# Kernel optimization log

Hardware: AMD Instinct MI355X
Metric: run time of the kernel (lower is better)

The kernel has to match this reference:

```python
import jax, jax.numpy as jnp
import numpy as np

_EPS = 1e-6
_ATTN_WIDTH = 64  # must match init_kwargs


def setup_inputs() -> dict:
    key = jax.random.key(0)
    k1, k2, k3, k4 = jax.random.split(key, 4)
    N, C, L, D = 8, 64, 512, 64
    scale = 1.0 / np.sqrt(C)
    return {
        "x": jax.random.normal(k1, (N, C, L), dtype=jnp.float32),
        "Wx": jax.random.normal(k2, (C, D), dtype=jnp.float32) * scale,
        "Wt": jax.random.normal(k3, (C, D), dtype=jnp.float32) * scale,
        "bh": jnp.zeros((D,), dtype=jnp.float32),
        "Wa": jax.random.normal(k4, (D, 1), dtype=jnp.float32) * scale,
        "ba": jnp.zeros((1,), dtype=jnp.float32),
    }


def reference(x, Wx, Wt, bh, Wa, ba):
    # x: (N, C, L) -> (N, L, C)
    xt = jnp.transpose(x, (0, 2, 1))
    q = jnp.einsum("nlc,cd->nld", xt, Wt)  # query proj
    k = jnp.einsum("nlc,cd->nld", xt, Wx)  # key proj
    # additive (Bahdanau) scores: h is (N, L, L, D)
    h = jnp.tanh(q[:, :, None, :] + k[:, None, :, :] + bh)
    e = jnp.einsum("nijd,d->nij", h, Wa[:, 0]) + ba[0]  # (N, L, L)
    e = jnp.exp(e - jnp.max(e, axis=-1, keepdims=True))
    # banded mask: keep where -attn_width//2 <= j-i <= attn_width//2 - 1
    L = e.shape[-1]
    i = jnp.arange(L)[:, None]
    j = jnp.arange(L)[None, :]
    d = j - i
    mask = (d >= -(_ATTN_WIDTH // 2)) & (d <= _ATTN_WIDTH // 2 - 1)
    e = jnp.where(mask, e, 0.0)
    s = jnp.sum(e, axis=-1, keepdims=True)
    a = e / (s + _EPS)  # (N, L, L)
    v = jnp.einsum("nij,njc->nic", a, xt)  # (N, L, C)
    v = jnp.transpose(v, (0, 2, 1))  # (N, C, L)
    return (v, a)
```

## Files before the change

kernel.cpp:

```cpp
#include <hip/hip_runtime.h>

#define N_ 8
#define C_ 64
#define L_ 512
#define D_ 64
#define TI 8
#define JT 71
#define KST 68
#define XST 76
#define XBST 88
#define AST 76

#define C2F 2.8853900817779268f

typedef _Float16 f16x8 __attribute__((ext_vector_type(8)));
typedef float    f32x4 __attribute__((ext_vector_type(4)));

__device__ __forceinline__ float rcp_f(float x) { return __builtin_amdgcn_rcpf(x); }
__device__ __forceinline__ float ex2(float x)   { return __builtin_amdgcn_exp2f(x); }

__global__ __launch_bounds__(512, 4) void fused_kernel(
    const float* __restrict__ x, const float* __restrict__ Wx,
    const float* __restrict__ Wt, const float* __restrict__ bh,
    const float* __restrict__ Wa,
    float* __restrict__ vout, float* __restrict__ aout)
{
  __shared__ __attribute__((aligned(16))) float    xs[C_ * XST];
  __shared__ __attribute__((aligned(16))) _Float16 xb[80 * XBST];
  __shared__ __attribute__((aligned(16))) float    k2b[96 * KST];
  __shared__ float ash[TI * AST];
  __shared__ float vs[C_][9];

  const int tid  = threadIdx.x;
  const int lane = tid & 63;
  const int bx   = blockIdx.x;
  const int n    = bx & 7;
  const int t    = bx >> 3;
  const int i0   = t << 3;
  const int jbase = i0 - 32;

  for (int idx = tid; idx < C_ * 18; idx += 512) {
    int c = idx / 18, qq = idx - c * 18;
    int jj = qq << 2;
    int j = jbase + jj;
    float4 xv = {0.f, 0.f, 0.f, 0.f};
    if (j >= 0 && j < L_) xv = *(const float4*)(x + (n * C_ + c) * L_ + j);
    *(float4*)&xs[c * XST + jj] = xv;
    _Float16* xbp = xb + c;
    xbp[(jj + 0) * XBST] = (_Float16)(xv.x * C2F);
    xbp[(jj + 1) * XBST] = (_Float16)(xv.y * C2F);
    xbp[(jj + 2) * XBST] = (_Float16)(xv.z * C2F);
    xbp[(jj + 3) * XBST] = (_Float16)(xv.w * C2F);
  }
  __syncthreads();

  const int w = __builtin_amdgcn_readfirstlane(tid >> 6);

  if (w < 6) {
    const int abase = (w < 5) ? w * 16 : 32;
    const float* Wm = (w < 5) ? Wx : Wt;
    const int l15 = lane & 15, g = lane >> 4;
    const _Float16* ap = xb + (abase + l15) * XBST + g * 8;
    const f16x8 af0 = *(const f16x8*)(ap);
    const f16x8 af1 = *(const f16x8*)(ap + 32);
    const int drow = ((w < 5) ? w * 16 : 80) + g * 4;
    #pragma unroll
    for (int nt = 0; nt < 4; ++nt) {
      f32x4 acc = {0.f, 0.f, 0.f, 0.f};
      #pragma unroll
      for (int kk = 0; kk < 2; ++kk) {
        const float* bp = Wm + (g * 8 + kk * 32) * D_ + nt * 16 + l15;
        f16x8 bf;
        bf[0] = (_Float16)bp[0 * D_];
        bf[1] = (_Float16)bp[1 * D_];
        bf[2] = (_Float16)bp[2 * D_];
        bf[3] = (_Float16)bp[3 * D_];
        bf[4] = (_Float16)bp[4 * D_];
        bf[5] = (_Float16)bp[5 * D_];
        bf[6] = (_Float16)bp[6 * D_];
        bf[7] = (_Float16)bp[7 * D_];
        acc = __builtin_amdgcn_mfma_f32_16x16x32_f16(kk ? af1 : af0, bf, acc, 0, 0, 0);
      }
      float* dp = &k2b[drow * KST + nt * 16 + l15];
      dp[0 * KST] = acc[0];
      dp[1 * KST] = acc[1];
      dp[2 * KST] = acc[2];
      dp[3 * KST] = acc[3];
    }
  }
  __syncthreads();
  k2b[(80 + w) * KST + lane] += bh[lane] * C2F;
  __syncthreads();

  const int i = i0 + w;
  const float* kp = &k2b[(w + lane) * KST];
  const float* qp = &k2b[(80 + w) * KST];
  float a0 = 0.f, a1 = 0.f, a2 = 0.f, a3 = 0.f;
  #pragma unroll 4
  for (int dc = 0; dc < D_; dc += 4) {
    float4 kv = *(const float4*)(kp + dc);
    float4 qv = *(const float4*)(qp + dc);
    float4 wv = *(const float4*)(Wa + dc);
    a0 = fmaf(rcp_f(ex2(kv.x + qv.x) + 1.f), wv.x, a0);
    a1 = fmaf(rcp_f(ex2(kv.y + qv.y) + 1.f), wv.y, a1);
    a2 = fmaf(rcp_f(ex2(kv.z + qv.z) + 1.f), wv.z, a2);
    a3 = fmaf(rcp_f(ex2(kv.w + qv.w) + 1.f), wv.w, a3);
  }
  const float acc = (a0 + a1) + (a2 + a3);

  const int j = i - 32 + lane;
  const bool valid = (j >= 0) && (j < L_);
  float m = valid ? acc : 1e30f;
  #pragma unroll
  for (int off = 32; off; off >>= 1) m = fminf(m, __shfl_xor(m, off, 64));
  float p = valid ? ex2(C2F * (m - acc)) : 0.f;
  float s = p;
  #pragma unroll
  for (int off = 32; off; off >>= 1) s += __shfl_xor(s, off, 64);
  const float av = p * rcp_f(s + 1e-6f);

  float* arow_s = &ash[w * AST];
  arow_s[lane] = 0.f;
  if (lane < AST - 64) arow_s[64 + lane] = 0.f;
  arow_s[w + lane] = av;

  {
    const int src  = (lane - i + 32) & 63;
    const float ar = __shfl(av, src, 64);
    const int jsrc = i - 32 + src;
    const int seg  = (jsrc >= 0) ? (jsrc >> 6) : 9;
    float* arow = aout + (size_t)(n * L_ + i) * L_;
    #pragma unroll
    for (int s8 = 0; s8 < 8; ++s8)
      arow[s8 * 64 + lane] = (s8 == seg) ? ar : 0.f;
  }

  {
    const int qstart = w & ~3;
    float v = 0.f;
    const float* xp = &xs[lane * XST];
    #pragma unroll 4
    for (int tq = 0; tq < 17; ++tq) {
      const int jj = qstart + 4 * tq;
      float4 a4 = *(const float4*)(arow_s + jj);
      float4 xq = *(const float4*)(xp + jj);
      v = fmaf(a4.x, xq.x, v);
      v = fmaf(a4.y, xq.y, v);
      v = fmaf(a4.z, xq.z, v);
      v = fmaf(a4.w, xq.w, v);
    }
    vs[lane][w] = v;
  }
  __syncthreads();
  {
    int c = tid >> 3, il = tid & 7;
    vout[((size_t)n * C_ + c) * L_ + i0 + il] = vs[c][il];
  }
}

extern "C" void kernel_launch(void* const* d_in, const int* in_sizes, int n_in,
                              void* d_out, int out_size, void* d_ws, size_t ws_size,
                              hipStream_t stream) {
  const float* x  = (const float*)d_in[0];
  const float* Wx = (const float*)d_in[1];
  const float* Wt = (const float*)d_in[2];
  const float* bh = (const float*)d_in[3];
  const float* Wa = (const float*)d_in[4];
  (void)d_ws; (void)ws_size;

  float* vout = (float*)d_out;
  float* aout = vout + N_ * C_ * L_;

  fused_kernel<<<512, 512, 0, stream>>>(x, Wx, Wt, bh, Wa, vout, aout);
}
```

Measured before the change: 15.26 us.

## Spread projection MFMAs across all waves and prefetch weights before barrier

Drops the separate fp16 transposed staging buffer and builds MFMA A-fragments straight from the fp32 x tile in shared memory. The 24 projection tiles are spread evenly over all 8 waves, 3 per wave, instead of 4 tiles on each of 6 waves. Weight loads are issued before the first barrier so they overlap the x tile loads. The bias is folded into the accumulator init, which removes one barrier and one read-modify-write pass. The cost is more register pressure from the prefetched weights and strided scalar LDS reads for the A fragments.

```diff
diff --git a/kernel.cpp b/kernel.cpp
--- a/kernel.cpp
+++ b/kernel.cpp
@@ -5,10 +5,8 @@
 #define L_ 512
 #define D_ 64
 #define TI 8
-#define JT 71
 #define KST 68
-#define XST 76
-#define XBST 88
+#define XST 84
 #define AST 76
 
 #define C2F 2.8853900817779268f
@@ -25,9 +23,8 @@
     const float* __restrict__ Wa,
     float* __restrict__ vout, float* __restrict__ aout)
 {
-  __shared__ __attribute__((aligned(16))) float    xs[C_ * XST];
-  __shared__ __attribute__((aligned(16))) _Float16 xb[80 * XBST];
-  __shared__ __attribute__((aligned(16))) float    k2b[96 * KST];
+  __shared__ __attribute__((aligned(16))) float xs[C_ * XST];
+  __shared__ __attribute__((aligned(16))) float k2b[96 * KST];
   __shared__ float ash[TI * AST];
   __shared__ float vs[C_][9];
 
@@ -39,57 +36,78 @@
   const int i0   = t << 3;
   const int jbase = i0 - 32;
 
-  for (int idx = tid; idx < C_ * 18; idx += 512) {
-    int c = idx / 18, qq = idx - c * 18;
-    int jj = qq << 2;
-    int j = jbase + jj;
-    float4 xv = {0.f, 0.f, 0.f, 0.f};
-    if (j >= 0 && j < L_) xv = *(const float4*)(x + (n * C_ + c) * L_ + j);
-    *(float4*)&xs[c * XST + jj] = xv;
-    _Float16* xbp = xb + c;
-    xbp[(jj + 0) * XBST] = (_Float16)(xv.x * C2F);
-    xbp[(jj + 1) * XBST] = (_Float16)(xv.y * C2F);
-    xbp[(jj + 2) * XBST] = (_Float16)(xv.z * C2F);
-    xbp[(jj + 3) * XBST] = (_Float16)(xv.w * C2F);
+  const int w   = __builtin_amdgcn_readfirstlane(tid >> 6);
+  const int l15 = lane & 15, g = lane >> 4;
+
+  float4 xv0 = {0.f,0.f,0.f,0.f}, xv1 = {0.f,0.f,0.f,0.f}, xv2 = {0.f,0.f,0.f,0.f};
+  int c0, c1, c2 = 0, jj0, jj1, jj2 = 0;
+  {
+    int idx = tid;        c0 = idx / 20; jj0 = (idx % 20) << 2;
+    int j = jbase + jj0;
+    if (j >= 0 && j < L_) xv0 = *(const float4*)(x + (n * C_ + c0) * L_ + j);
   }
+  {
+    int idx = tid + 512;  c1 = idx / 20; jj1 = (idx % 20) << 2;
+    int j = jbase + jj1;
+    if (j >= 0 && j < L_) xv1 = *(const float4*)(x + (n * C_ + c1) * L_ + j);
+  }
+  if (tid < 256) {
+    int idx = tid + 1024; c2 = idx / 20; jj2 = (idx % 20) << 2;
+    int j = jbase + jj2;
+    if (j >= 0 && j < L_) xv2 = *(const float4*)(x + (n * C_ + c2) * L_ + j);
+  }
+
+  float bpre[3][2][8];
+  #pragma unroll
+  for (int u3 = 0; u3 < 3; ++u3) {
+    const int u = w * 3 + u3, mt = u >> 2, nt = u & 3;
+    const float* Wm = (mt < 5) ? Wx : Wt;
+    #pragma unroll
+    for (int kk = 0; kk < 2; ++kk)
+      #pragma unroll
+      for (int e = 0; e < 8; ++e)
+        bpre[u3][kk][e] = Wm[(g * 8 + kk * 32 + e) * D_ + nt * 16 + l15];
+  }
+
+  *(float4*)&xs[c0 * XST + jj0] = xv0;
+  *(float4*)&xs[c1 * XST + jj1] = xv1;
+  if (tid < 256) *(float4*)&xs[c2 * XST + jj2] = xv2;
+
+  f16x8 b16[3][2];
+  #pragma unroll
+  for (int u3 = 0; u3 < 3; ++u3)
+    #pragma unroll
+    for (int kk = 0; kk < 2; ++kk)
+      #pragma unroll
+      for (int e = 0; e < 8; ++e)
+        b16[u3][kk][e] = (_Float16)bpre[u3][kk][e];
+
   __syncthreads();
 
-  const int w = __builtin_amdgcn_readfirstlane(tid >> 6);
-
-  if (w < 6) {
-    const int abase = (w < 5) ? w * 16 : 32;
-    const float* Wm = (w < 5) ? Wx : Wt;
-    const int l15 = lane & 15, g = lane >> 4;
-    const _Float16* ap = xb + (abase + l15) * XBST + g * 8;
-    const f16x8 af0 = *(const f16x8*)(ap);
-    const f16x8 af1 = *(const f16x8*)(ap + 32);
-    const int drow = ((w < 5) ? w * 16 : 80) + g * 4;
+  #pragma unroll
+  for (int u3 = 0; u3 < 3; ++u3) {
+    const int u = w * 3 + u3, mt = u >> 2, nt = u & 3;
+    const int abase = (mt < 5) ? mt * 16 : 32;
+    const int drow  = ((mt < 5) ? mt * 16 : 80) + g * 4;
+    f16x8 af0, af1;
     #pragma unroll
-    for (int nt = 0; nt < 4; ++nt) {
-      f32x4 acc = {0.f, 0.f, 0.f, 0.f};
-      #pragma unroll
-      for (int kk = 0; kk < 2; ++kk) {
-        const float* bp = Wm + (g * 8 + kk * 32) * D_ + nt * 16 + l15;
-        f16x8 bf;
-        bf[0] = (_Float16)bp[0 * D_];
-        bf[1] = (_Float16)bp[1 * D_];
-        bf[2] = (_Float16)bp[2 * D_];
-        bf[3] = (_Float16)bp[3 * D_];
-        bf[4] = (_Float16)bp[4 * D_];
-        bf[5] = (_Float16)bp[5 * D_];
-        bf[6] = (_Float16)bp[6 * D_];
-        bf[7] = (_Float16)bp[7 * D_];
-        acc = __builtin_amdgcn_mfma_f32_16x16x32_f16(kk ? af1 : af0, bf, acc, 0, 0, 0);
-      }
-      float* dp = &k2b[drow * KST + nt * 16 + l15];
-      dp[0 * KST] = acc[0];
-      dp[1 * KST] = acc[1];
-      dp[2 * KST] = acc[2];
-      dp[3 * KST] = acc[3];
+    for (int e = 0; e < 8; ++e) {
+      af0[e] = (_Float16)(xs[(g * 8 + e) * XST + abase + l15] * C2F);
+      af1[e] = (_Float16)(xs[(g * 8 + e + 32) * XST + abase + l15] * C2F);
     }
+    f32x4 acc = {0.f, 0.f, 0.f, 0.f};
+    if (mt == 5) {
+      float b = bh[nt * 16 + l15] * C2F;
+      acc[0] = b; acc[1] = b; acc[2] = b; acc[3] = b;
+    }
+    acc = __builtin_amdgcn_mfma_f32_16x16x32_f16(af0, b16[u3][0], acc, 0, 0, 0);
+    acc = __builtin_amdgcn_mfma_f32_16x16x32_f16(af1, b16[u3][1], acc, 0, 0, 0);
+    float* dp = &k2b[drow * KST + nt * 16 + l15];
+    dp[0]       = acc[0];
+    dp[KST]     = acc[1];
+    dp[2 * KST] = acc[2];
+    dp[3 * KST] = acc[3];
   }
-  __syncthreads();
-  k2b[(80 + w) * KST + lane] += bh[lane] * C2F;
   __syncthreads();
 
   const int i = i0 + w;
```

Result: slower. 16.07 us (+5.3%).

## Halve query rows per block and restructure projection MFMA work across waves

Applied to the files above, without the earlier changes.

Each block now handles 4 query rows with 256 threads, and the grid grows to 1024 blocks. Each wave owns one 16-column slice of the key/query projections and reuses its weight fragments across all row tiles. The query bias is folded into the MFMA accumulator init, which removes one sync. The fp32 x tile is dropped, so the value product now reads the fp16 x copy (no longer pre-scaled). This cuts shared memory and adds parallelism, at the cost of more redundant halo loads per output row and lower precision in the value accumulation.

```diff
diff --git a/kernel.cpp b/kernel.cpp
--- a/kernel.cpp
+++ b/kernel.cpp
@@ -3,11 +3,8 @@
 #define N_ 8
 #define C_ 64
 #define L_ 512
-#define D_ 64
-#define TI 8
-#define JT 71
+#define TI 4
 #define KST 68
-#define XST 76
 #define XBST 88
 #define AST 76
 
@@ -19,85 +16,95 @@
 __device__ __forceinline__ float rcp_f(float x) { return __builtin_amdgcn_rcpf(x); }
 __device__ __forceinline__ float ex2(float x)   { return __builtin_amdgcn_exp2f(x); }
 
-__global__ __launch_bounds__(512, 4) void fused_kernel(
+__global__ __launch_bounds__(256, 4) void fused_kernel(
     const float* __restrict__ x, const float* __restrict__ Wx,
     const float* __restrict__ Wt, const float* __restrict__ bh,
     const float* __restrict__ Wa,
     float* __restrict__ vout, float* __restrict__ aout)
 {
-  __shared__ __attribute__((aligned(16))) float    xs[C_ * XST];
   __shared__ __attribute__((aligned(16))) _Float16 xb[80 * XBST];
-  __shared__ __attribute__((aligned(16))) float    k2b[96 * KST];
-  __shared__ float ash[TI * AST];
-  __shared__ float vs[C_][9];
+  __shared__ __attribute__((aligned(16))) float k2b[72 * KST];
+  __shared__ __attribute__((aligned(16))) float ash[TI * AST];
+  __shared__ float vs[C_ * 5];
 
   const int tid  = threadIdx.x;
   const int lane = tid & 63;
   const int bx   = blockIdx.x;
   const int n    = bx & 7;
   const int t    = bx >> 3;
-  const int i0   = t << 3;
+  const int i0   = t << 2;
   const int jbase = i0 - 32;
 
-  for (int idx = tid; idx < C_ * 18; idx += 512) {
-    int c = idx / 18, qq = idx - c * 18;
-    int jj = qq << 2;
+  const int w   = __builtin_amdgcn_readfirstlane(tid >> 6);
+  const int l15 = lane & 15, g = lane >> 4;
+
+  for (int idx = tid; idx < C_ * 17; idx += 256) {
+    int c = idx / 17, q = idx - c * 17;
+    int jj = q << 2;
     int j = jbase + jj;
     float4 xv = {0.f, 0.f, 0.f, 0.f};
     if (j >= 0 && j < L_) xv = *(const float4*)(x + (n * C_ + c) * L_ + j);
-    *(float4*)&xs[c * XST + jj] = xv;
-    _Float16* xbp = xb + c;
-    xbp[(jj + 0) * XBST] = (_Float16)(xv.x * C2F);
-    xbp[(jj + 1) * XBST] = (_Float16)(xv.y * C2F);
-    xbp[(jj + 2) * XBST] = (_Float16)(xv.z * C2F);
-    xbp[(jj + 3) * XBST] = (_Float16)(xv.w * C2F);
+    _Float16* p = xb + c;
+    p[(jj + 0) * XBST] = (_Float16)xv.x;
+    p[(jj + 1) * XBST] = (_Float16)xv.y;
+    p[(jj + 2) * XBST] = (_Float16)xv.z;
+    p[(jj + 3) * XBST] = (_Float16)xv.w;
   }
   __syncthreads();
 
-  const int w = __builtin_amdgcn_readfirstlane(tid >> 6);
-
-  if (w < 6) {
-    const int abase = (w < 5) ? w * 16 : 32;
-    const float* Wm = (w < 5) ? Wx : Wt;
-    const int l15 = lane & 15, g = lane >> 4;
-    const _Float16* ap = xb + (abase + l15) * XBST + g * 8;
-    const f16x8 af0 = *(const f16x8*)(ap);
-    const f16x8 af1 = *(const f16x8*)(ap + 32);
-    const int drow = ((w < 5) ? w * 16 : 80) + g * 4;
+  {
+    const int nt = w;
+    f16x8 bx16[2], bt16[2];
     #pragma unroll
-    for (int nt = 0; nt < 4; ++nt) {
+    for (int kk = 0; kk < 2; ++kk)
+      #pragma unroll
+      for (int e = 0; e < 8; ++e) {
+        const int krow = g * 8 + kk * 32 + e;
+        bx16[kk][e] = (_Float16)(Wx[krow * 64 + nt * 16 + l15] * C2F);
+        bt16[kk][e] = (_Float16)(Wt[krow * 64 + nt * 16 + l15] * C2F);
+      }
+    #pragma unroll
+    for (int mt = 0; mt < 5; ++mt) {
+      const _Float16* ap = xb + (mt * 16 + l15) * XBST + g * 8;
+      const f16x8 af0 = *(const f16x8*)(ap);
+      const f16x8 af1 = *(const f16x8*)(ap + 32);
       f32x4 acc = {0.f, 0.f, 0.f, 0.f};
-      #pragma unroll
-      for (int kk = 0; kk < 2; ++kk) {
-        const float* bp = Wm + (g * 8 + kk * 32) * D_ + nt * 16 + l15;
-        f16x8 bf;
-        bf[0] = (_Float16)bp[0 * D_];
-        bf[1] = (_Float16)bp[1 * D_];
-        bf[2] = (_Float16)bp[2 * D_];
-        bf[3] = (_Float16)bp[3 * D_];
-        bf[4] = (_Float16)bp[4 * D_];
-        bf[5] = (_Float16)bp[5 * D_];
-        bf[6] = (_Float16)bp[6 * D_];
-        bf[7] = (_Float16)bp[7 * D_];
-        acc = __builtin_amdgcn_mfma_f32_16x16x32_f16(kk ? af1 : af0, bf, acc, 0, 0, 0);
+      acc = __builtin_amdgcn_mfma_f32_16x16x32_f16(af0, bx16[0], acc, 0, 0, 0);
+      acc = __builtin_amdgcn_mfma_f32_16x16x32_f16(af1, bx16[1], acc, 0, 0, 0);
+      float* dp = &k2b[(mt * 16 + g * 4) * KST + nt * 16 + l15];
+      if (mt < 4) {
+        dp[0]       = acc[0];
+        dp[KST]     = acc[1];
+        dp[2 * KST] = acc[2];
+        dp[3 * KST] = acc[3];
+      } else if (g == 0) {
+        dp[0]       = acc[0];
+        dp[KST]     = acc[1];
+        dp[2 * KST] = acc[2];
       }
-      float* dp = &k2b[drow * KST + nt * 16 + l15];
-      dp[0 * KST] = acc[0];
-      dp[1 * KST] = acc[1];
-      dp[2 * KST] = acc[2];
-      dp[3 * KST] = acc[3];
+      if (mt == 2) {
+        const float b = bh[nt * 16 + l15] * C2F;
+        f32x4 qa = {b, b, b, b};
+        qa = __builtin_amdgcn_mfma_f32_16x16x32_f16(af0, bt16[0], qa, 0, 0, 0);
+        qa = __builtin_amdgcn_mfma_f32_16x16x32_f16(af1, bt16[1], qa, 0, 0, 0);
+        if (g == 0) {
+          float* qp = &k2b[68 * KST + nt * 16 + l15];
+          qp[0]       = qa[0];
+          qp[KST]     = qa[1];
+          qp[2 * KST] = qa[2];
+          qp[3 * KST] = qa[3];
+        }
+      }
     }
   }
-  __syncthreads();
-  k2b[(80 + w) * KST + lane] += bh[lane] * C2F;
   __syncthreads();
 
   const int i = i0 + w;
   const float* kp = &k2b[(w + lane) * KST];
-  const float* qp = &k2b[(80 + w) * KST];
+  const float* qp = &k2b[(68 + w) * KST];
   float a0 = 0.f, a1 = 0.f, a2 = 0.f, a3 = 0.f;
   #pragma unroll 4
-  for (int dc = 0; dc < D_; dc += 4) {
+  for (int dc = 0; dc < 64; dc += 4) {
     float4 kv = *(const float4*)(kp + dc);
     float4 qv = *(const float4*)(qp + dc);
     float4 wv = *(const float4*)(Wa + dc);
@@ -136,25 +143,18 @@
   }
 
   {
-    const int qstart = w & ~3;
     float v = 0.f;
-    const float* xp = &xs[lane * XST];
+    const _Float16* xp = xb + lane;
+    const float* as4 = &ash[w * AST];
     #pragma unroll 4
-    for (int tq = 0; tq < 17; ++tq) {
-      const int jj = qstart + 4 * tq;
-      float4 a4 = *(const float4*)(arow_s + jj);
-      float4 xq = *(const float4*)(xp + jj);
-      v = fmaf(a4.x, xq.x, v);
-      v = fmaf(a4.y, xq.y, v);
-      v = fmaf(a4.z, xq.z, v);
-      v = fmaf(a4.w, xq.w, v);
-    }
-    vs[lane][w] = v;
+    for (int jj = 0; jj < 68; ++jj)
+      v = fmaf(as4[jj], (float)xp[jj * XBST], v);
+    vs[lane * 5 + w] = v;
   }
   __syncthreads();
   {
-    int c = tid >> 3, il = tid & 7;
-    vout[((size_t)n * C_ + c) * L_ + i0 + il] = vs[c][il];
+    int c = tid >> 2, il = tid & 3;
+    vout[((size_t)n * C_ + c) * L_ + i0 + il] = vs[c * 5 + il];
   }
 }
 
@@ -171,5 +171,5 @@
   float* vout = (float*)d_out;
   float* aout = vout + N_ * C_ * L_;
 
-  fused_kernel<<<512, 512, 0, stream>>>(x, Wx, Wt, bh, Wa, vout, aout);
+  fused_kernel<<<1024, 256, 0, stream>>>(x, Wx, Wt, bh, Wa, vout, aout);
 }
```

Result: slower. 16.45 us (+7.7%).
